# Kernel optimization log

Measured on AMD Instinct MI355X. Metric: run time of the kernel, lower is better.

Reference implementation:

```python
import jax, jax.numpy as jnp
import numpy as np

N_NODES = 10000
N_MOTIFS = 2500          # N_NODES / subgraph_size(=4)
N_AUG = N_NODES + N_MOTIFS
N_EDGES = 500000
NFEAT = 512
NHID = 128


def setup_inputs() -> dict:
    key = jax.random.key(0)
    ks = jax.random.split(key, 14)
    s = 0.05  # param init scale
    return {
        "x": jax.random.normal(ks[0], (N_NODES, NFEAT), jnp.float32),
        "edge_index": jax.random.randint(ks[1], (2, N_EDGES), 0, N_AUG, jnp.int64),
        "motif_list": jax.random.randint(ks[2], (N_MOTIFS, 4), 0, N_NODES, jnp.int64),
        "W1": jax.random.normal(ks[3], (NFEAT, 2 * NHID), jnp.float32) * s,
        "a_src1": jax.random.normal(ks[4], (2 * NHID,), jnp.float32) * s,
        "a_dst1": jax.random.normal(ks[5], (2 * NHID,), jnp.float32) * s,
        "b1": jnp.zeros((2 * NHID,), jnp.float32),
        "W2": jax.random.normal(ks[6], (2 * NHID, NHID), jnp.float32) * s,
        "a_src2": jax.random.normal(ks[7], (NHID,), jnp.float32) * s,
        "a_dst2": jax.random.normal(ks[8], (NHID,), jnp.float32) * s,
        "b2": jnp.zeros((NHID,), jnp.float32),
        "W_lin": jax.random.normal(ks[9], (NFEAT, NHID), jnp.float32) * s,  # torch Linear(nhid, nfeat) weight
        "b_lin": jnp.zeros((NFEAT,), jnp.float32),
    }


def gat_layer(x, src, dst, W, a_s, a_d, b, n):
    """Single-head GATConv (PyG semantics): edge-softmax attention over dst."""
    h = x @ W                                              # [n, out]
    alpha_s = h @ a_s                                      # [n]
    alpha_d = h @ a_d                                      # [n]
    e = jax.nn.leaky_relu(alpha_s[src] + alpha_d[dst], 0.2)  # [E]
    m = jax.ops.segment_max(e, dst, num_segments=n)        # stable softmax per dst
    w = jnp.exp(e - m[dst])
    denom = jax.ops.segment_sum(w, dst, num_segments=n)
    coef = w / (denom[dst] + 1e-16)                        # [E]
    out = jax.ops.segment_sum(coef[:, None] * h[src], dst, num_segments=n)
    return out + b


def reference(x, edge_index, motif_list, W1, a_src1, a_dst1, b1,
              W2, a_src2, a_dst2, b2, W_lin, b_lin):
    n = x.shape[0] + motif_list.shape[0]
    # augmented features: mean of each motif's node features appended as motif nodes
    x_aug = jnp.concatenate([x, jnp.mean(x[motif_list], axis=1)], axis=0)  # [N_AUG, F]
    # augmented edge list + self loops (GATConv adds self loops)
    loops = jnp.arange(n, dtype=edge_index.dtype)
    src = jnp.concatenate([edge_index[0], loops])
    dst = jnp.concatenate([edge_index[1], loops])
    h1 = gat_layer(x_aug, src, dst, W1, a_src1, a_dst1, b1, n)   # [N_AUG, 2*NHID]
    h2 = gat_layer(h1, src, dst, W2, a_src2, a_dst2, b2, n)      # [N_AUG, NHID]
    rec_adj = jax.nn.sigmoid(h2 @ h2.T)                          # [N_AUG, N_AUG]
    rec_feature = jax.nn.sigmoid(h2 @ W_lin.T + b_lin)           # [N_AUG, NFEAT]
    return (rec_feature, rec_adj)
```

## Files before the change

### kernel.cpp

```cpp
#include <hip/hip_runtime.h>

typedef unsigned short u16;
typedef unsigned int   u32;
typedef __attribute__((ext_vector_type(8))) short short8;
typedef __attribute__((ext_vector_type(4))) float f32x4;

#define N_NODES 10000
#define N_MOTIFS 2500
#define N_AUG   12500
#define N_EDGES 500000
#define E_TOT   512500
#define NFEAT   512
#define NH1     256
#define NH2     128

__device__ __forceinline__ float b2f(u16 u){ return __uint_as_float(((u32)u) << 16); }
__device__ __forceinline__ u16 f2b(float f){
  u32 x = __float_as_uint(f);
  x += 0x7fffu + ((x >> 16) & 1u);
  return (u16)(x >> 16);
}

#define PREP_Z   (N_AUG + 8)
#define PREP_W1  (NFEAT * NH1)
#define PREP_W2  (NH1 * NH2)
#define PREP_WL  (NFEAT * NH2)
#define PREP_B   (NH2)
#define PREP_TOT (PREP_Z + PREP_W1 + PREP_W2 + PREP_WL + PREP_B)

__global__ void k_prep(const float* __restrict__ W1, const float* __restrict__ W2,
                       const float* __restrict__ Wl, const float* __restrict__ b1,
                       int* __restrict__ cnt,
                       u16* __restrict__ W1T, u16* __restrict__ W2T, u16* __restrict__ Wlb,
                       float* __restrict__ b1W2){
  int i = blockIdx.x * blockDim.x + threadIdx.x;
  if (i < PREP_Z){ cnt[i] = 0; return; }
  i -= PREP_Z;
  if (i < PREP_W1){
    int r = i / NH1, c = i - r * NH1;
    W1T[(size_t)c * NFEAT + r] = f2b(W1[i]);
    return;
  }
  i -= PREP_W1;
  if (i < PREP_W2){
    int r = i / NH2, c = i - r * NH2;
    W2T[(size_t)c * NH1 + r] = f2b(W2[i]);
    return;
  }
  i -= PREP_W2;
  if (i < PREP_WL){ Wlb[i] = f2b(Wl[i]); return; }
  i -= PREP_WL;
  if (i < PREP_B){
    float s = 0.f;
    #pragma unroll 8
    for (int k = 0; k < NH1; ++k) s += b1[k] * W2[(size_t)k * NH2 + i];
    b1W2[i] = s;
  }
}

__global__ void k_xaug(const float* __restrict__ x, const int* __restrict__ motif,
                       u16* __restrict__ xb){
  int gid = blockIdx.x * blockDim.x + threadIdx.x;
  int row = gid >> 6;
  int c   = (gid & 63) << 3;
  if (row >= N_AUG) return;
  float v[8];
  if (row < N_NODES){
    const float* s = &x[(size_t)row * NFEAT + c];
    #pragma unroll
    for (int k = 0; k < 8; ++k) v[k] = s[k];
  } else {
    int m = row - N_NODES;
    const float* p0 = &x[(size_t)motif[m*4+0] * NFEAT + c];
    const float* p1 = &x[(size_t)motif[m*4+1] * NFEAT + c];
    const float* p2 = &x[(size_t)motif[m*4+2] * NFEAT + c];
    const float* p3 = &x[(size_t)motif[m*4+3] * NFEAT + c];
    #pragma unroll
    for (int k = 0; k < 8; ++k) v[k] = (p0[k] + p1[k] + p2[k] + p3[k]) * 0.25f;
  }
  short8 o;
  #pragma unroll
  for (int k = 0; k < 8; ++k) o[k] = (short)f2b(v[k]);
  *(short8*)&xb[(size_t)row * NFEAT + c] = o;
}

__global__ void k_hist(const int* __restrict__ ei, int* __restrict__ cnt){
  int i = blockIdx.x * blockDim.x + threadIdx.x;
  if (i >= E_TOT) return;
  int d = (i < N_EDGES) ? ei[N_EDGES + i] : (i - N_EDGES);
  atomicAdd(&cnt[d], 1);
}

__global__ void k_scan(const int* __restrict__ cnt, int* __restrict__ offs, int* __restrict__ cur){
  __shared__ int part[1024];
  int t = threadIdx.x;
  const int CH = 13;
  int base = t * CH;
  int s = 0;
  for (int i = 0; i < CH; ++i){ int idx = base + i; if (idx < N_AUG) s += cnt[idx]; }
  part[t] = s;
  __syncthreads();
  for (int off = 1; off < 1024; off <<= 1){
    int v = 0;
    if (t >= off) v = part[t - off];
    __syncthreads();
    if (t >= off) part[t] += v;
    __syncthreads();
  }
  int run = (t == 0) ? 0 : part[t - 1];
  for (int i = 0; i < CH; ++i){
    int idx = base + i;
    if (idx <= N_AUG){
      offs[idx] = run;
      if (idx < N_AUG){ cur[idx] = run; run += cnt[idx]; }
    }
  }
}

__global__ void k_scatter(const int* __restrict__ ei, int* __restrict__ cur, int* __restrict__ srcs){
  int i = blockIdx.x * blockDim.x + threadIdx.x;
  if (i >= E_TOT) return;
  int s, d;
  if (i < N_EDGES){ s = ei[i]; d = ei[N_EDGES + i]; } else { s = i - N_EDGES; d = s; }
  int pos = atomicAdd(&cur[d], 1);
  srcs[pos] = s;
}

template<int DIM>
__global__ void k_alpha(const u16* __restrict__ h, const float* __restrict__ avs,
                        const float* __restrict__ avd, float* __restrict__ oS, float* __restrict__ oD){
  __shared__ float shS[8], shD[8];
  int n = blockIdx.x, t = threadIdx.x;
  int lane = t & 63, wid = t >> 6;
  float hv = b2f(h[(size_t)n * DIM + t]);
  float s = hv * avs[t];
  float d = hv * avd[t];
  #pragma unroll
  for (int o = 32; o; o >>= 1){ s += __shfl_down(s, o); d += __shfl_down(d, o); }
  if (lane == 0){ shS[wid] = s; shD[wid] = d; }
  __syncthreads();
  if (t == 0){
    float ss = 0.f, dd = 0.f;
    #pragma unroll
    for (int i = 0; i < DIM/64; ++i){ ss += shS[i]; dd += shD[i]; }
    oS[n] = ss; oD[n] = dd;
  }
}

__global__ __launch_bounds__(64) void k_agg128(
    const int* __restrict__ offs, const int* __restrict__ srcs,
    const float* __restrict__ aS, const float* __restrict__ aD,
    const u16* __restrict__ hb, const float* __restrict__ bias,
    u16* __restrict__ hout){
  __shared__ float wsh[128];
  __shared__ int   ssh[128];
  int d = blockIdx.x, t = threadIdx.x;
  int r0 = offs[d], r1 = offs[d + 1];
  float adv = aD[d];

  float a0 = 0.f, a1 = 0.f, smp = 0.f;
  for (int base = r0; base < r1; base += 128){
    int cntE = min(128, r1 - base);
    __syncthreads();
    for (int j = t; j < cntE; j += 64){
      int s = srcs[base + j];
      ssh[j] = s;
      float e = aS[s] + adv;
      e = (e >= 0.f) ? e : 0.2f * e;
      float w = __expf(e);
      wsh[j] = w;
      smp += w;
    }
    __syncthreads();
    #pragma unroll 4
    for (int j = 0; j < cntE; ++j){
      u32 v = *(const u32*)&hb[(size_t)ssh[j] * NH2 + 2*t];
      float w = wsh[j];
      a0 = fmaf(w, b2f((u16)(v & 0xffffu)), a0);
      a1 = fmaf(w, b2f((u16)(v >> 16)), a1);
    }
  }
  #pragma unroll
  for (int o = 32; o; o >>= 1) smp += __shfl_down(smp, o);
  smp = __shfl(smp, 0);
  float inv = 1.f / (smp + 1e-16f);
  float o0 = a0 * inv + bias[2*t];
  float o1 = a1 * inv + bias[2*t + 1];
  u32 pv = (u32)f2b(o0) | ((u32)f2b(o1) << 16);
  *(u32*)&hout[(size_t)d * NH2 + 2*t] = pv;
}

__global__ __launch_bounds__(256) void k_adj(const u16* __restrict__ H,
                                             float* __restrict__ C){
  __shared__ float stage[64][132];
  int t = threadIdx.x;
  int lane = t & 63, wid = t >> 6;
  int wm = wid >> 1, wn = wid & 1;
  int li = lane & 15, lg = lane >> 4;
  int m0 = blockIdx.y * 128, n0 = blockIdx.x * 128;

  const u16* arow[4];
  const u16* brow[4];
  #pragma unroll
  for (int i = 0; i < 4; ++i){
    int gm = m0 + wm*64 + i*16 + li; if (gm >= N_AUG) gm = N_AUG - 1;
    arow[i] = &H[(size_t)gm * NH2];
    int gn = n0 + wn*64 + i*16 + li; if (gn >= N_AUG) gn = N_AUG - 1;
    brow[i] = &H[(size_t)gn * NH2];
  }

  f32x4 acc[4][4];
  #pragma unroll
  for (int i = 0; i < 4; ++i)
    #pragma unroll
    for (int j = 0; j < 4; ++j)
      acc[i][j] = {0.f, 0.f, 0.f, 0.f};

  #pragma unroll 1
  for (int kq = 0; kq < 4; ++kq){
    int col = kq*32 + lg*8;
    short8 af[4], bfr[4];
    #pragma unroll
    for (int mi = 0; mi < 4; ++mi) af[mi]  = *(const short8*)&arow[mi][col];
    #pragma unroll
    for (int ni = 0; ni < 4; ++ni) bfr[ni] = *(const short8*)&brow[ni][col];
    #pragma unroll
    for (int mi = 0; mi < 4; ++mi)
      #pragma unroll
      for (int ni = 0; ni < 4; ++ni)
        acc[mi][ni] = __builtin_amdgcn_mfma_f32_16x16x32_bf16(af[mi], bfr[ni], acc[mi][ni], 0, 0, 0);
  }

  #pragma unroll
  for (int half = 0; half < 2; ++half){
    __syncthreads();
    if (wm == half){
      #pragma unroll
      for (int mi = 0; mi < 4; ++mi)
        #pragma unroll
        for (int ni = 0; ni < 4; ++ni){
          int col = wn*64 + ni*16 + li;
          #pragma unroll
          for (int r = 0; r < 4; ++r){
            float v = acc[mi][ni][r];
            stage[mi*16 + lg*4 + r][col] = 1.f / (1.f + __expf(-v));
          }
        }
    }
    __syncthreads();
    #pragma unroll
    for (int pss = 0; pss < 8; ++pss){
      int flat = pss * 1024 + t * 4;
      int lr = flat >> 7, c = flat & 127;
      int gm = m0 + half*64 + lr;
      if (gm >= N_AUG) continue;
      int gn = n0 + c;
      f32x4 v = *(const f32x4*)&stage[lr][c];
      if (gn + 3 < N_AUG){
        *(f32x4*)&C[(size_t)gm * N_AUG + gn] = v;
      } else {
        #pragma unroll
        for (int e = 0; e < 4; ++e)
          if (gn + e < N_AUG) C[(size_t)gm * N_AUG + gn + e] = v[e];
      }
    }
  }
}

template<int EPI>
__global__ __launch_bounds__(256) void k_gemm(
    const u16* __restrict__ A, const u16* __restrict__ B,
    void* __restrict__ Cv, const float* __restrict__ bias,
    int M, int N, int K){
  __shared__ union SM {
    struct { u16 As[128][72]; u16 Bs[128][72]; } ab;
    float stage[64][132];
  } sm;
  int t = threadIdx.x;
  int lane = t & 63, wid = t >> 6;
  int wm = wid >> 1, wn = wid & 1;
  int m0 = blockIdx.y * 128, n0 = blockIdx.x * 128;

  f32x4 acc[4][4];
  #pragma unroll
  for (int i = 0; i < 4; ++i)
    #pragma unroll
    for (int j = 0; j < 4; ++j)
      acc[i][j] = {0.f, 0.f, 0.f, 0.f};

  for (int k0 = 0; k0 < K; k0 += 64){
    __syncthreads();
    #pragma unroll
    for (int i = 0; i < 4; ++i){
      int id = t + i * 256;
      int r = id >> 3, c = (id & 7) << 3;
      int gm = m0 + r; if (gm >= M) gm = M - 1;
      int gn = n0 + r; if (gn >= N) gn = N - 1;
      *(short8*)&sm.ab.As[r][c] = *(const short8*)&A[(size_t)gm * K + k0 + c];
      *(short8*)&sm.ab.Bs[r][c] = *(const short8*)&B[(size_t)gn * K + k0 + c];
    }
    __syncthreads();
    #pragma unroll
    for (int kk = 0; kk < 2; ++kk){
      int kof = kk * 32 + (lane >> 4) * 8;
      short8 af[4], bfr[4];
      #pragma unroll
      for (int mi = 0; mi < 4; ++mi) af[mi]  = *(const short8*)&sm.ab.As[wm*64 + mi*16 + (lane & 15)][kof];
      #pragma unroll
      for (int ni = 0; ni < 4; ++ni) bfr[ni] = *(const short8*)&sm.ab.Bs[wn*64 + ni*16 + (lane & 15)][kof];
      #pragma unroll
      for (int mi = 0; mi < 4; ++mi)
        #pragma unroll
        for (int ni = 0; ni < 4; ++ni)
          acc[mi][ni] = __builtin_amdgcn_mfma_f32_16x16x32_bf16(af[mi], bfr[ni], acc[mi][ni], 0, 0, 0);
    }
  }

  if (EPI == 0){
    u16* C = (u16*)Cv;
    #pragma unroll
    for (int mi = 0; mi < 4; ++mi)
      #pragma unroll
      for (int ni = 0; ni < 4; ++ni){
        int gn = n0 + wn*64 + ni*16 + (lane & 15);
        if (gn >= N) continue;
        #pragma unroll
        for (int r = 0; r < 4; ++r){
          int gm = m0 + wm*64 + mi*16 + (lane >> 4)*4 + r;
          if (gm >= M) continue;
          C[(size_t)gm * N + gn] = f2b(acc[mi][ni][r]);
        }
      }
  } else {
    float* C = (float*)Cv;
    #pragma unroll
    for (int half = 0; half < 2; ++half){
      __syncthreads();
      if (wm == half){
        #pragma unroll
        for (int mi = 0; mi < 4; ++mi)
          #pragma unroll
          for (int ni = 0; ni < 4; ++ni){
            int col = wn*64 + ni*16 + (lane & 15);
            int gn  = n0 + col;
            int gnc = (gn < N) ? gn : (N - 1);
            #pragma unroll
            for (int r = 0; r < 4; ++r){
              int lrow = mi*16 + (lane >> 4)*4 + r;
              float v = acc[mi][ni][r];
              if (EPI == 2) v += bias[gnc];
              v = 1.f / (1.f + __expf(-v));
              sm.stage[lrow][col] = v;
            }
          }
      }
      __syncthreads();
      #pragma unroll
      for (int pss = 0; pss < 8; ++pss){
        int flat = pss * 1024 + t * 4;
        int lr = flat >> 7, c = flat & 127;
        int gm = m0 + half*64 + lr;
        if (gm >= M) continue;
        int gn = n0 + c;
        f32x4 v = *(const f32x4*)&sm.stage[lr][c];
        if (gn + 3 < N){
          *(f32x4*)&C[(size_t)gm * N + gn] = v;
        } else {
          #pragma unroll
          for (int e = 0; e < 4; ++e)
            if (gn + e < N) C[(size_t)gm * N + gn + e] = v[e];
        }
      }
    }
  }
}

extern "C" void kernel_launch(void* const* d_in, const int* in_sizes, int n_in,
                              void* d_out, int out_size, void* d_ws, size_t ws_size,
                              hipStream_t stream){
  const float* x    = (const float*)d_in[0];
  const int*   ei   = (const int*)d_in[1];
  const int*   mot  = (const int*)d_in[2];
  const float* W1   = (const float*)d_in[3];
  const float* a_s1 = (const float*)d_in[4];
  const float* a_d1 = (const float*)d_in[5];
  const float* b1   = (const float*)d_in[6];
  const float* W2   = (const float*)d_in[7];
  const float* a_s2 = (const float*)d_in[8];
  const float* a_d2 = (const float*)d_in[9];
  const float* b2   = (const float*)d_in[10];
  const float* Wl   = (const float*)d_in[11];
  const float* bl   = (const float*)d_in[12];

  char* p = (char*)d_ws;
  auto alloc = [&](size_t bytes){ void* r = (void*)p; p += (bytes + 255) & ~(size_t)255; return r; };
  u16*   xaugb  = (u16*)alloc((size_t)N_AUG * NFEAT * 2);
  u16*   W1T    = (u16*)alloc((size_t)NH1 * NFEAT * 2);
  u16*   W2T    = (u16*)alloc((size_t)NH2 * NH1 * 2);
  u16*   Wlb    = (u16*)alloc((size_t)NFEAT * NH2 * 2);
  u16*   h1b    = (u16*)alloc((size_t)N_AUG * NH1 * 2);
  u16*   g      = (u16*)alloc((size_t)N_AUG * NH2 * 2);
  u16*   h2preb = (u16*)alloc((size_t)N_AUG * NH2 * 2);
  u16*   h2o    = (u16*)alloc((size_t)N_AUG * NH2 * 2);
  float* aS     = (float*)alloc((size_t)N_AUG * 4);
  float* aD     = (float*)alloc((size_t)N_AUG * 4);
  float* b1W2   = (float*)alloc((size_t)NH2 * 4);
  int*   cnt    = (int*)alloc((size_t)(N_AUG + 8) * 4);
  int*   offs   = (int*)alloc((size_t)(N_AUG + 8) * 4);
  int*   cur    = (int*)alloc((size_t)(N_AUG + 8) * 4);
  int*   srcs   = (int*)alloc((size_t)E_TOT * 4);

  float* out_feat = (float*)d_out;
  float* out_adj  = out_feat + (size_t)N_AUG * NFEAT;

  k_prep<<<(PREP_TOT + 255) / 256, 256, 0, stream>>>(W1, W2, Wl, b1, cnt, W1T, W2T, Wlb, b1W2);
  k_xaug<<<(N_AUG * 64 + 255) / 256, 256, 0, stream>>>(x, mot, xaugb);
  k_hist<<<(E_TOT + 255) / 256, 256, 0, stream>>>(ei, cnt);
  k_scan<<<1, 1024, 0, stream>>>(cnt, offs, cur);
  k_scatter<<<(E_TOT + 255) / 256, 256, 0, stream>>>(ei, cur, srcs);

  { dim3 gr(NH1 / 128, 98); k_gemm<0><<<gr, 256, 0, stream>>>(xaugb, W1T, h1b, nullptr, N_AUG, NH1, NFEAT); }
  k_alpha<NH1><<<N_AUG, NH1, 0, stream>>>(h1b, a_s1, a_d1, aS, aD);
  { dim3 gr(1, 98); k_gemm<0><<<gr, 256, 0, stream>>>(h1b, W2T, g, nullptr, N_AUG, NH2, NH1); }
  k_agg128<<<N_AUG, 64, 0, stream>>>(offs, srcs, aS, aD, g, b1W2, h2preb);

  k_alpha<NH2><<<N_AUG, NH2, 0, stream>>>(h2preb, a_s2, a_d2, aS, aD);
  k_agg128<<<N_AUG, 64, 0, stream>>>(offs, srcs, aS, aD, h2preb, b2, h2o);

  { dim3 gr(NFEAT / 128, 98); k_gemm<2><<<gr, 256, 0, stream>>>(h2o, Wlb, out_feat, bl, N_AUG, NFEAT, NH2); }
  { dim3 gr(98, 98); k_adj<<<gr, 256, 0, stream>>>(h2o, out_adj); }
}
```

Baseline: 449.3 us.

## Keep A fragments in registers and loop k_adj over eight column tiles

Each k_adj block now loads its 128-row A slice of H into registers once, then iterates over up to eight 128-column output tiles. The grid shrinks from 98x98 to 13x98 blocks. This cuts redundant A loads and per-block launch and setup overhead. In exchange it raises register pressure from the 16 held fragments and leaves far fewer blocks to fill the GPU, while the kernel stays dominated by the write bandwidth of the large fp32 output.

```diff
diff --git a/kernel.cpp b/kernel.cpp
--- a/kernel.cpp
+++ b/kernel.cpp
@@ -197,71 +197,83 @@
   int lane = t & 63, wid = t >> 6;
   int wm = wid >> 1, wn = wid & 1;
   int li = lane & 15, lg = lane >> 4;
-  int m0 = blockIdx.y * 128, n0 = blockIdx.x * 128;
-
-  const u16* arow[4];
-  const u16* brow[4];
+  int m0 = blockIdx.y * 128;
+  int nb = blockIdx.x * 1024;
+
+  short8 af[4][4];
   #pragma unroll
-  for (int i = 0; i < 4; ++i){
-    int gm = m0 + wm*64 + i*16 + li; if (gm >= N_AUG) gm = N_AUG - 1;
-    arow[i] = &H[(size_t)gm * NH2];
-    int gn = n0 + wn*64 + i*16 + li; if (gn >= N_AUG) gn = N_AUG - 1;
-    brow[i] = &H[(size_t)gn * NH2];
-  }
-
-  f32x4 acc[4][4];
-  #pragma unroll
-  for (int i = 0; i < 4; ++i)
-    #pragma unroll
-    for (int j = 0; j < 4; ++j)
-      acc[i][j] = {0.f, 0.f, 0.f, 0.f};
+  for (int mi = 0; mi < 4; ++mi){
+    int gm = m0 + wm*64 + mi*16 + li; if (gm >= N_AUG) gm = N_AUG - 1;
+    const u16* ar = &H[(size_t)gm * NH2];
+    #pragma unroll
+    for (int kq = 0; kq < 4; ++kq)
+      af[kq][mi] = *(const short8*)&ar[kq*32 + lg*8];
+  }
 
   #pragma unroll 1
-  for (int kq = 0; kq < 4; ++kq){
-    int col = kq*32 + lg*8;
-    short8 af[4], bfr[4];
-    #pragma unroll
-    for (int mi = 0; mi < 4; ++mi) af[mi]  = *(const short8*)&arow[mi][col];
-    #pragma unroll
-    for (int ni = 0; ni < 4; ++ni) bfr[ni] = *(const short8*)&brow[ni][col];
-    #pragma unroll
-    for (int mi = 0; mi < 4; ++mi)
-      #pragma unroll
-      for (int ni = 0; ni < 4; ++ni)
-        acc[mi][ni] = __builtin_amdgcn_mfma_f32_16x16x32_bf16(af[mi], bfr[ni], acc[mi][ni], 0, 0, 0);
-  }
-
-  #pragma unroll
-  for (int half = 0; half < 2; ++half){
-    __syncthreads();
-    if (wm == half){
+  for (int ct = 0; ct < 8; ++ct){
+    int n0 = nb + ct * 128;
+    if (n0 >= N_AUG) break;
+
+    const u16* brow[4];
+    #pragma unroll
+    for (int ni = 0; ni < 4; ++ni){
+      int gn = n0 + wn*64 + ni*16 + li; if (gn >= N_AUG) gn = N_AUG - 1;
+      brow[ni] = &H[(size_t)gn * NH2];
+    }
+
+    f32x4 acc[4][4];
+    #pragma unroll
+    for (int i = 0; i < 4; ++i)
+      #pragma unroll
+      for (int j = 0; j < 4; ++j)
+        acc[i][j] = {0.f, 0.f, 0.f, 0.f};
+
+    #pragma unroll
+    for (int kq = 0; kq < 4; ++kq){
+      int col = kq*32 + lg*8;
+      short8 bfr[4];
+      #pragma unroll
+      for (int ni = 0; ni < 4; ++ni) bfr[ni] = *(const short8*)&brow[ni][col];
       #pragma unroll
       for (int mi = 0; mi < 4; ++mi)
         #pragma unroll
-        for (int ni = 0; ni < 4; ++ni){
-          int col = wn*64 + ni*16 + li;
+        for (int ni = 0; ni < 4; ++ni)
+          acc[mi][ni] = __builtin_amdgcn_mfma_f32_16x16x32_bf16(af[kq][mi], bfr[ni], acc[mi][ni], 0, 0, 0);
+    }
+
+    #pragma unroll
+    for (int half = 0; half < 2; ++half){
+      __syncthreads();
+      if (wm == half){
+        #pragma unroll
+        for (int mi = 0; mi < 4; ++mi)
           #pragma unroll
-          for (int r = 0; r < 4; ++r){
-            float v = acc[mi][ni][r];
-            stage[mi*16 + lg*4 + r][col] = 1.f / (1.f + __expf(-v));
+          for (int ni = 0; ni < 4; ++ni){
+            int col = wn*64 + ni*16 + li;
+            #pragma unroll
+            for (int r = 0; r < 4; ++r){
+              float v = acc[mi][ni][r];
+              stage[mi*16 + lg*4 + r][col] = 1.f / (1.f + __expf(-v));
+            }
           }
+      }
+      __syncthreads();
+      #pragma unroll
+      for (int pss = 0; pss < 8; ++pss){
+        int flat = pss * 1024 + t * 4;
+        int lr = flat >> 7, c = flat & 127;
+        int gm = m0 + half*64 + lr;
+        if (gm >= N_AUG) continue;
+        int gn = n0 + c;
+        f32x4 v = *(const f32x4*)&stage[lr][c];
+        if (gn + 3 < N_AUG){
+          *(f32x4*)&C[(size_t)gm * N_AUG + gn] = v;
+        } else {
+          #pragma unroll
+          for (int e = 0; e < 4; ++e)
+            if (gn + e < N_AUG) C[(size_t)gm * N_AUG + gn + e] = v[e];
         }
-    }
-    __syncthreads();
-    #pragma unroll
-    for (int pss = 0; pss < 8; ++pss){
-      int flat = pss * 1024 + t * 4;
-      int lr = flat >> 7, c = flat & 127;
-      int gm = m0 + half*64 + lr;
-      if (gm >= N_AUG) continue;
-      int gn = n0 + c;
-      f32x4 v = *(const f32x4*)&stage[lr][c];
-      if (gn + 3 < N_AUG){
-        *(f32x4*)&C[(size_t)gm * N_AUG + gn] = v;
-      } else {
-        #pragma unroll
-        for (int e = 0; e < 4; ++e)
-          if (gn + e < N_AUG) C[(size_t)gm * N_AUG + gn + e] = v[e];
       }
     }
   }
@@ -428,5 +440,5 @@
   k_agg128<<<N_AUG, 64, 0, stream>>>(offs, srcs, aS, aD, h2preb, b2, h2o);
 
   { dim3 gr(NFEAT / 128, 98); k_gemm<2><<<gr, 256, 0, stream>>>(h2o, Wlb, out_feat, bl, N_AUG, NFEAT, NH2); }
-  { dim3 gr(98, 98); k_adj<<<gr, 256, 0, stream>>>(h2o, out_adj); }
-}
+  { dim3 gr(13, 98); k_adj<<<gr, 256, 0, stream>>>(h2o, out_adj); }
+}
```

Result: slower. 537.0 us (+19.5%).

## Merge independent kernels into combined launches and stage adj GEMM through LDS

Applied to the files above, without the earlier changes.

Combines weight prep with x augmentation, the second GEMM with the layer-1 alpha computation, and the feature and adjacency output GEMMs into single launches that pick their role by block index. The adjacency kernel now loads tiles through shared memory like the generic GEMM instead of reading fragments straight from global memory. The goal is fewer launches and gaps between small kernels. The cost is heterogeneous blocks in one grid and the added LDS staging in the dominant adjacency kernel.

```diff
diff --git a/kernel.cpp b/kernel.cpp
--- a/kernel.cpp
+++ b/kernel.cpp
@@ -21,46 +21,49 @@
   return (u16)(x >> 16);
 }
 
-#define PREP_Z   (N_AUG + 8)
-#define PREP_W1  (NFEAT * NH1)
-#define PREP_W2  (NH1 * NH2)
-#define PREP_WL  (NFEAT * NH2)
-#define PREP_B   (NH2)
-#define PREP_TOT (PREP_Z + PREP_W1 + PREP_W2 + PREP_WL + PREP_B)
-
-__global__ void k_prep(const float* __restrict__ W1, const float* __restrict__ W2,
-                       const float* __restrict__ Wl, const float* __restrict__ b1,
-                       int* __restrict__ cnt,
-                       u16* __restrict__ W1T, u16* __restrict__ W2T, u16* __restrict__ Wlb,
-                       float* __restrict__ b1W2){
-  int i = blockIdx.x * blockDim.x + threadIdx.x;
-  if (i < PREP_Z){ cnt[i] = 0; return; }
-  i -= PREP_Z;
-  if (i < PREP_W1){
-    int r = i / NH1, c = i - r * NH1;
-    W1T[(size_t)c * NFEAT + r] = f2b(W1[i]);
+#define PREP_Z    (N_AUG + 8)
+#define PREP_W1   (NFEAT * NH1)
+#define PREP_W2   (NH1 * NH2)
+#define PREP_WL   (NFEAT * NH2)
+#define PREP_B    (NH2)
+#define PREP_TOT  (PREP_Z + PREP_W1 + PREP_W2 + PREP_WL + PREP_B)
+#define PREP_BLKS ((PREP_TOT + 255) / 256)
+#define XAUG_BLKS ((N_AUG * 64 + 255) / 256)
+
+__global__ void k_prepx(const float* __restrict__ W1, const float* __restrict__ W2,
+                        const float* __restrict__ Wl, const float* __restrict__ b1,
+                        const float* __restrict__ x, const int* __restrict__ motif,
+                        int* __restrict__ cnt,
+                        u16* __restrict__ W1T, u16* __restrict__ W2T, u16* __restrict__ Wlb,
+                        float* __restrict__ b1W2, u16* __restrict__ xb){
+  int bid = blockIdx.x, t = threadIdx.x;
+  if (bid < PREP_BLKS){
+    int i = bid * 256 + t;
+    if (i < PREP_Z){ cnt[i] = 0; return; }
+    i -= PREP_Z;
+    if (i < PREP_W1){
+      int r = i / NH1, c = i - r * NH1;
+      W1T[(size_t)c * NFEAT + r] = f2b(W1[i]);
+      return;
+    }
+    i -= PREP_W1;
+    if (i < PREP_W2){
+      int r = i / NH2, c = i - r * NH2;
+      W2T[(size_t)c * NH1 + r] = f2b(W2[i]);
+      return;
+    }
+    i -= PREP_W2;
+    if (i < PREP_WL){ Wlb[i] = f2b(Wl[i]); return; }
+    i -= PREP_WL;
+    if (i < PREP_B){
+      float s = 0.f;
+      #pragma unroll 8
+      for (int k = 0; k < NH1; ++k) s += b1[k] * W2[(size_t)k * NH2 + i];
+      b1W2[i] = s;
+    }
     return;
   }
-  i -= PREP_W1;
-  if (i < PREP_W2){
-    int r = i / NH2, c = i - r * NH2;
-    W2T[(size_t)c * NH1 + r] = f2b(W2[i]);
-    return;
-  }
-  i -= PREP_W2;
-  if (i < PREP_WL){ Wlb[i] = f2b(Wl[i]); return; }
-  i -= PREP_WL;
-  if (i < PREP_B){
-    float s = 0.f;
-    #pragma unroll 8
-    for (int k = 0; k < NH1; ++k) s += b1[k] * W2[(size_t)k * NH2 + i];
-    b1W2[i] = s;
-  }
-}
-
-__global__ void k_xaug(const float* __restrict__ x, const int* __restrict__ motif,
-                       u16* __restrict__ xb){
-  int gid = blockIdx.x * blockDim.x + threadIdx.x;
+  int gid = (bid - PREP_BLKS) * 256 + t;
   int row = gid >> 6;
   int c   = (gid & 63) << 3;
   if (row >= N_AUG) return;
@@ -190,92 +193,15 @@
   *(u32*)&hout[(size_t)d * NH2 + 2*t] = pv;
 }
 
-__global__ __launch_bounds__(256) void k_adj(const u16* __restrict__ H,
-                                             float* __restrict__ C){
-  __shared__ float stage[64][132];
-  int t = threadIdx.x;
-  int lane = t & 63, wid = t >> 6;
-  int wm = wid >> 1, wn = wid & 1;
-  int li = lane & 15, lg = lane >> 4;
-  int m0 = blockIdx.y * 128, n0 = blockIdx.x * 128;
-
-  const u16* arow[4];
-  const u16* brow[4];
-  #pragma unroll
-  for (int i = 0; i < 4; ++i){
-    int gm = m0 + wm*64 + i*16 + li; if (gm >= N_AUG) gm = N_AUG - 1;
-    arow[i] = &H[(size_t)gm * NH2];
-    int gn = n0 + wn*64 + i*16 + li; if (gn >= N_AUG) gn = N_AUG - 1;
-    brow[i] = &H[(size_t)gn * NH2];
-  }
-
-  f32x4 acc[4][4];
-  #pragma unroll
-  for (int i = 0; i < 4; ++i)
-    #pragma unroll
-    for (int j = 0; j < 4; ++j)
-      acc[i][j] = {0.f, 0.f, 0.f, 0.f};
-
-  #pragma unroll 1
-  for (int kq = 0; kq < 4; ++kq){
-    int col = kq*32 + lg*8;
-    short8 af[4], bfr[4];
-    #pragma unroll
-    for (int mi = 0; mi < 4; ++mi) af[mi]  = *(const short8*)&arow[mi][col];
-    #pragma unroll
-    for (int ni = 0; ni < 4; ++ni) bfr[ni] = *(const short8*)&brow[ni][col];
-    #pragma unroll
-    for (int mi = 0; mi < 4; ++mi)
-      #pragma unroll
-      for (int ni = 0; ni < 4; ++ni)
-        acc[mi][ni] = __builtin_amdgcn_mfma_f32_16x16x32_bf16(af[mi], bfr[ni], acc[mi][ni], 0, 0, 0);
-  }
-
-  #pragma unroll
-  for (int half = 0; half < 2; ++half){
-    __syncthreads();
-    if (wm == half){
-      #pragma unroll
-      for (int mi = 0; mi < 4; ++mi)
-        #pragma unroll
-        for (int ni = 0; ni < 4; ++ni){
-          int col = wn*64 + ni*16 + li;
-          #pragma unroll
-          for (int r = 0; r < 4; ++r){
-            float v = acc[mi][ni][r];
-            stage[mi*16 + lg*4 + r][col] = 1.f / (1.f + __expf(-v));
-          }
-        }
-    }
-    __syncthreads();
-    #pragma unroll
-    for (int pss = 0; pss < 8; ++pss){
-      int flat = pss * 1024 + t * 4;
-      int lr = flat >> 7, c = flat & 127;
-      int gm = m0 + half*64 + lr;
-      if (gm >= N_AUG) continue;
-      int gn = n0 + c;
-      f32x4 v = *(const f32x4*)&stage[lr][c];
-      if (gn + 3 < N_AUG){
-        *(f32x4*)&C[(size_t)gm * N_AUG + gn] = v;
-      } else {
-        #pragma unroll
-        for (int e = 0; e < 4; ++e)
-          if (gn + e < N_AUG) C[(size_t)gm * N_AUG + gn + e] = v[e];
-      }
-    }
-  }
-}
-
-template<int EPI>
-__global__ __launch_bounds__(256) void k_gemm(
+union SMU {
+  struct { u16 As[128][72]; u16 Bs[128][72]; } ab;
+  float stage[64][132];
+};
+
+__global__ __launch_bounds__(256) void k_gemm0(
     const u16* __restrict__ A, const u16* __restrict__ B,
-    void* __restrict__ Cv, const float* __restrict__ bias,
-    int M, int N, int K){
-  __shared__ union SM {
-    struct { u16 As[128][72]; u16 Bs[128][72]; } ab;
-    float stage[64][132];
-  } sm;
+    u16* __restrict__ C, int M, int N, int K){
+  __shared__ SMU sm;
   int t = threadIdx.x;
   int lane = t & 63, wid = t >> 6;
   int wm = wid >> 1, wn = wid & 1;
@@ -315,9 +241,65 @@
           acc[mi][ni] = __builtin_amdgcn_mfma_f32_16x16x32_bf16(af[mi], bfr[ni], acc[mi][ni], 0, 0, 0);
     }
   }
-
-  if (EPI == 0){
-    u16* C = (u16*)Cv;
+  #pragma unroll
+  for (int mi = 0; mi < 4; ++mi)
+    #pragma unroll
+    for (int ni = 0; ni < 4; ++ni){
+      int gn = n0 + wn*64 + ni*16 + (lane & 15);
+      if (gn >= N) continue;
+      #pragma unroll
+      for (int r = 0; r < 4; ++r){
+        int gm = m0 + wm*64 + mi*16 + (lane >> 4)*4 + r;
+        if (gm >= M) continue;
+        C[(size_t)gm * N + gn] = f2b(acc[mi][ni][r]);
+      }
+    }
+}
+
+__global__ __launch_bounds__(256) void k_g2a(
+    const u16* __restrict__ h1b, const u16* __restrict__ W2T, u16* __restrict__ g,
+    const float* __restrict__ avs, const float* __restrict__ avd,
+    float* __restrict__ oS, float* __restrict__ oD){
+  __shared__ SMU sm;
+  int bid = blockIdx.x, t = threadIdx.x;
+  int lane = t & 63, wid = t >> 6;
+  if (bid < 98){
+    int wm = wid >> 1, wn = wid & 1;
+    int m0 = bid * 128, n0 = 0;
+    const int M = N_AUG, N = NH2, K = NH1;
+    f32x4 acc[4][4];
+    #pragma unroll
+    for (int i = 0; i < 4; ++i)
+      #pragma unroll
+      for (int j = 0; j < 4; ++j)
+        acc[i][j] = {0.f, 0.f, 0.f, 0.f};
+    for (int k0 = 0; k0 < K; k0 += 64){
+      __syncthreads();
+      #pragma unroll
+      for (int i = 0; i < 4; ++i){
+        int id = t + i * 256;
+        int r = id >> 3, c = (id & 7) << 3;
+        int gm = m0 + r; if (gm >= M) gm = M - 1;
+        int gn = n0 + r; if (gn >= N) gn = N - 1;
+        *(short8*)&sm.ab.As[r][c] = *(const short8*)&h1b[(size_t)gm * K + k0 + c];
+        *(short8*)&sm.ab.Bs[r][c] = *(const short8*)&W2T[(size_t)gn * K + k0 + c];
+      }
+      __syncthreads();
+      #pragma unroll
+      for (int kk = 0; kk < 2; ++kk){
+        int kof = kk * 32 + (lane >> 4) * 8;
+        short8 af[4], bfr[4];
+        #pragma unroll
+        for (int mi = 0; mi < 4; ++mi) af[mi]  = *(const short8*)&sm.ab.As[wm*64 + mi*16 + (lane & 15)][kof];
+        #pragma unroll
+        for (int ni = 0; ni < 4; ++ni) bfr[ni] = *(const short8*)&sm.ab.Bs[wn*64 + ni*16 + (lane & 15)][kof];
+        #pragma unroll
+        for (int mi = 0; mi < 4; ++mi)
+          #pragma unroll
+          for (int ni = 0; ni < 4; ++ni)
+            acc[mi][ni] = __builtin_amdgcn_mfma_f32_16x16x32_bf16(af[mi], bfr[ni], acc[mi][ni], 0, 0, 0);
+      }
+    }
     #pragma unroll
     for (int mi = 0; mi < 4; ++mi)
       #pragma unroll
@@ -328,48 +310,123 @@
         for (int r = 0; r < 4; ++r){
           int gm = m0 + wm*64 + mi*16 + (lane >> 4)*4 + r;
           if (gm >= M) continue;
-          C[(size_t)gm * N + gn] = f2b(acc[mi][ni][r]);
+          g[(size_t)gm * N + gn] = f2b(acc[mi][ni][r]);
         }
       }
   } else {
-    float* C = (float*)Cv;
-    #pragma unroll
-    for (int half = 0; half < 2; ++half){
-      __syncthreads();
-      if (wm == half){
-        #pragma unroll
-        for (int mi = 0; mi < 4; ++mi)
+    int n = bid - 98;
+    float* shS = (float*)&sm;
+    float* shD = shS + 8;
+    float hv = b2f(h1b[(size_t)n * NH1 + t]);
+    float s = hv * avs[t];
+    float d = hv * avd[t];
+    #pragma unroll
+    for (int o = 32; o; o >>= 1){ s += __shfl_down(s, o); d += __shfl_down(d, o); }
+    if (lane == 0){ shS[wid] = s; shD[wid] = d; }
+    __syncthreads();
+    if (t == 0){
+      float ss = 0.f, dd = 0.f;
+      #pragma unroll
+      for (int i = 0; i < 4; ++i){ ss += shS[i]; dd += shD[i]; }
+      oS[n] = ss; oD[n] = dd;
+    }
+  }
+}
+
+#define ADJ_BLKS (98 * 98)
+#define FEAT_BLKS (4 * 98)
+__global__ __launch_bounds__(256) void k_tail(
+    const u16* __restrict__ H, const u16* __restrict__ Wlb, const float* __restrict__ bl,
+    float* __restrict__ out_adj, float* __restrict__ out_feat){
+  __shared__ SMU sm;
+  int bid = blockIdx.x, t = threadIdx.x;
+  int lane = t & 63, wid = t >> 6;
+  int wm = wid >> 1, wn = wid & 1;
+
+  const u16* B; float* C; int N, m0, n0; bool ub;
+  if (bid < ADJ_BLKS){
+    B = H; C = out_adj; N = N_AUG; ub = false;
+    int bx = bid % 98, by = bid / 98;
+    m0 = by * 128; n0 = bx * 128;
+  } else {
+    int f = bid - ADJ_BLKS;
+    B = Wlb; C = out_feat; N = 512; ub = true;
+    m0 = (f >> 2) * 128; n0 = (f & 3) * 128;
+  }
+  const int M = N_AUG, K = NH2;
+
+  f32x4 acc[4][4];
+  #pragma unroll
+  for (int i = 0; i < 4; ++i)
+    #pragma unroll
+    for (int j = 0; j < 4; ++j)
+      acc[i][j] = {0.f, 0.f, 0.f, 0.f};
+
+  #pragma unroll
+  for (int k0 = 0; k0 < K; k0 += 64){
+    __syncthreads();
+    #pragma unroll
+    for (int i = 0; i < 4; ++i){
+      int id = t + i * 256;
+      int r = id >> 3, c = (id & 7) << 3;
+      int gm = m0 + r; if (gm >= M) gm = M - 1;
+      int gn = n0 + r; if (gn >= N) gn = N - 1;
+      *(short8*)&sm.ab.As[r][c] = *(const short8*)&H[(size_t)gm * K + k0 + c];
+      *(short8*)&sm.ab.Bs[r][c] = *(const short8*)&B[(size_t)gn * K + k0 + c];
+    }
+    __syncthreads();
+    #pragma unroll
+    for (int kk = 0; kk < 2; ++kk){
+      int kof = kk * 32 + (lane >> 4) * 8;
+      short8 af[4], bfr[4];
+      #pragma unroll
+      for (int mi = 0; mi < 4; ++mi) af[mi]  = *(const short8*)&sm.ab.As[wm*64 + mi*16 + (lane & 15)][kof];
+      #pragma unroll
+      for (int ni = 0; ni < 4; ++ni) bfr[ni] = *(const short8*)&sm.ab.Bs[wn*64 + ni*16 + (lane & 15)][kof];
+      #pragma unroll
+      for (int mi = 0; mi < 4; ++mi)
+        #pragma unroll
+        for (int ni = 0; ni < 4; ++ni)
+          acc[mi][ni] = __builtin_amdgcn_mfma_f32_16x16x32_bf16(af[mi], bfr[ni], acc[mi][ni], 0, 0, 0);
+    }
+  }
+
+  #pragma unroll
+  for (int half = 0; half < 2; ++half){
+    __syncthreads();
+    if (wm == half){
+      #pragma unroll
+      for (int mi = 0; mi < 4; ++mi)
+        #pragma unroll
+        for (int ni = 0; ni < 4; ++ni){
+          int col = wn*64 + ni*16 + (lane & 15);
+          int gn  = n0 + col;
+          int gnc = (gn < N) ? gn : (N - 1);
           #pragma unroll
-          for (int ni = 0; ni < 4; ++ni){
-            int col = wn*64 + ni*16 + (lane & 15);
-            int gn  = n0 + col;
-            int gnc = (gn < N) ? gn : (N - 1);
-            #pragma unroll
-            for (int r = 0; r < 4; ++r){
-              int lrow = mi*16 + (lane >> 4)*4 + r;
-              float v = acc[mi][ni][r];
-              if (EPI == 2) v += bias[gnc];
-              v = 1.f / (1.f + __expf(-v));
-              sm.stage[lrow][col] = v;
-            }
+          for (int r = 0; r < 4; ++r){
+            int lrow = mi*16 + (lane >> 4)*4 + r;
+            float v = acc[mi][ni][r];
+            if (ub) v += bl[gnc];
+            v = 1.f / (1.f + __expf(-v));
+            sm.stage[lrow][col] = v;
           }
-      }
-      __syncthreads();
-      #pragma unroll
-      for (int pss = 0; pss < 8; ++pss){
-        int flat = pss * 1024 + t * 4;
-        int lr = flat >> 7, c = flat & 127;
-        int gm = m0 + half*64 + lr;
-        if (gm >= M) continue;
-        int gn = n0 + c;
-        f32x4 v = *(const f32x4*)&sm.stage[lr][c];
-        if (gn + 3 < N){
-          *(f32x4*)&C[(size_t)gm * N + gn] = v;
-        } else {
-          #pragma unroll
-          for (int e = 0; e < 4; ++e)
-            if (gn + e < N) C[(size_t)gm * N + gn + e] = v[e];
         }
+    }
+    __syncthreads();
+    #pragma unroll
+    for (int pss = 0; pss < 8; ++pss){
+      int flat = pss * 1024 + t * 4;
+      int lr = flat >> 7, c = flat & 127;
+      int gm = m0 + half*64 + lr;
+      if (gm >= M) continue;
+      int gn = n0 + c;
+      f32x4 v = *(const f32x4*)&sm.stage[lr][c];
+      if (gn + 3 < N){
+        *(f32x4*)&C[(size_t)gm * N + gn] = v;
+      } else {
+        #pragma unroll
+        for (int e = 0; e < 4; ++e)
+          if (gn + e < N) C[(size_t)gm * N + gn + e] = v[e];
       }
     }
   }
@@ -413,20 +470,18 @@
   float* out_feat = (float*)d_out;
   float* out_adj  = out_feat + (size_t)N_AUG * NFEAT;
 
-  k_prep<<<(PREP_TOT + 255) / 256, 256, 0, stream>>>(W1, W2, Wl, b1, cnt, W1T, W2T, Wlb, b1W2);
-  k_xaug<<<(N_AUG * 64 + 255) / 256, 256, 0, stream>>>(x, mot, xaugb);
+  k_prepx<<<PREP_BLKS + XAUG_BLKS, 256, 0, stream>>>(W1, W2, Wl, b1, x, mot,
+                                                     cnt, W1T, W2T, Wlb, b1W2, xaugb);
   k_hist<<<(E_TOT + 255) / 256, 256, 0, stream>>>(ei, cnt);
   k_scan<<<1, 1024, 0, stream>>>(cnt, offs, cur);
   k_scatter<<<(E_TOT + 255) / 256, 256, 0, stream>>>(ei, cur, srcs);
 
-  { dim3 gr(NH1 / 128, 98); k_gemm<0><<<gr, 256, 0, stream>>>(xaugb, W1T, h1b, nullptr, N_AUG, NH1, NFEAT); }
-  k_alpha<NH1><<<N_AUG, NH1, 0, stream>>>(h1b, a_s1, a_d1, aS, aD);
-  { dim3 gr(1, 98); k_gemm<0><<<gr, 256, 0, stream>>>(h1b, W2T, g, nullptr, N_AUG, NH2, NH1); }
+  { dim3 gr(NH1 / 128, 98); k_gemm0<<<gr, 256, 0, stream>>>(xaugb, W1T, h1b, N_AUG, NH1, NFEAT); }
+  k_g2a<<<98 + N_AUG, 256, 0, stream>>>(h1b, W2T, g, a_s1, a_d1, aS, aD);
   k_agg128<<<N_AUG, 64, 0, stream>>>(offs, srcs, aS, aD, g, b1W2, h2preb);
 
   k_alpha<NH2><<<N_AUG, NH2, 0, stream>>>(h2preb, a_s2, a_d2, aS, aD);
   k_agg128<<<N_AUG, 64, 0, stream>>>(offs, srcs, aS, aD, h2preb, b2, h2o);
 
-  { dim3 gr(NFEAT / 128, 98); k_gemm<2><<<gr, 256, 0, stream>>>(h2o, Wlb, out_feat, bl, N_AUG, NFEAT, NH2); }
-  { dim3 gr(98, 98); k_adj<<<gr, 256, 0, stream>>>(h2o, out_adj); }
-}
+  k_tail<<<ADJ_BLKS + FEAT_BLKS, 256, 0, stream>>>(h2o, Wlb, bl, out_adj, out_feat);
+}
```

Result: slower. 488.3 us (+8.7%).
